# Optimization experiments

Measured on AMD Instinct MI355X. Metric: run time of the kernel, lower is better.

Reference implementation:

```python
import jax, jax.numpy as jnp
import numpy as np

N, E, DIN, DH, DC = 50000, 1600000, 128, 128, 40
EPS = 1e-5  # BatchNorm eps


def _seg_sum(v, idx, n):
    return jax.ops.segment_sum(v, idx, num_segments=n)


def setup_inputs() -> dict:
    key = jax.random.key(0)
    ks = jax.random.split(key, 24)
    rn = lambda i, shp, s=0.05: jax.random.normal(ks[i], shp, jnp.float32) * s
    return {
        "x": jax.random.normal(ks[0], (N, DIN), jnp.float32),
        "src": jax.random.randint(ks[1], (E,), 0, N, jnp.int32),
        "dst": jax.random.randint(ks[2], (E,), 0, N, jnp.int32),
        # CoNet layer 1 (in -> hidden)
        "w11s": rn(3, (DIN, DH)), "w11n": rn(4, (DIN, DH)), "b11": jnp.zeros((DH,), jnp.float32),
        "w12": rn(5, (DIN, DH)), "b12": jnp.zeros((DH,), jnp.float32),
        "w13": rn(6, (DIN, DH)), "a13l": rn(7, (DH,)), "a13r": rn(8, (DH,)), "b13": jnp.zeros((DH,), jnp.float32),
        "cw1": jax.random.uniform(ks[9], (3,), jnp.float32, 0.5, 1.5),
        # BatchNorm1d
        "g": jnp.ones((DH,), jnp.float32), "be": jnp.zeros((DH,), jnp.float32),
        # CoNet layer 2 (hidden -> out)
        "w21s": rn(10, (DH, DC)), "w21n": rn(11, (DH, DC)), "b21": jnp.zeros((DC,), jnp.float32),
        "w22": rn(12, (DH, DC)), "b22": jnp.zeros((DC,), jnp.float32),
        "w23": rn(13, (DH, DC)), "a23l": rn(14, (DC,)), "a23r": rn(15, (DC,)), "b23": jnp.zeros((DC,), jnp.float32),
        "cw2": jax.random.uniform(ks[16], (3,), jnp.float32, 0.5, 1.5),
    }


def conet(x, src, dst, ws, wn, bs, wg, bg, wa, al, ar, ba, cw):
    """AFFN CoNet: SAGE(mean) + GCN + GAT(1 head), fused by normalized weights."""
    n = x.shape[0]
    ones = jnp.ones((src.shape[0],), x.dtype)
    indeg = _seg_sum(ones, dst, n)   # in-degree per node
    outdeg = _seg_sum(ones, src, n)  # out-degree per node

    # --- SAGEConv, mean aggregator: fc_self(x) + fc_neigh(mean_neigh(x)) ---
    nei = _seg_sum(x[src], dst, n) / jnp.maximum(indeg, 1.0)[:, None]
    x1 = x @ ws + nei @ wn + bs

    ns = jnp.maximum(outdeg, 1.0) ** -0.5
    nd = jnp.maximum(indeg, 1.0) ** -0.5
    h = _seg_sum((x * ns[:, None])[src], dst, n) * nd[:, None]
    x2 = h @ wg + bg

    # --- GATConv, 1 head ---
    f = x @ wa                       # [N, out]
    el = f @ al                      # [N]
    er = f @ ar                      # [N]
    e = jax.nn.leaky_relu(el[src] + er[dst], 0.2)  # [E]
    m = jax.ops.segment_max(e, dst, num_segments=n)
    a = jnp.exp(e - m[dst])
    s = _seg_sum(a, dst, n)
    alpha = a / jnp.maximum(s[dst], 1e-9)
    x3 = _seg_sum(alpha[:, None] * f[src], dst, n) + ba

    w = cw / jnp.sum(cw)
    return w[0] * x1 + w[1] * x2 + w[2] * x3


def reference(x, src, dst,
              w11s, w11n, b11, w12, b12, w13, a13l, a13r, b13, cw1,
              g, be,
              w21s, w21n, b21, w22, b22, w23, a23l, a23r, b23, cw2):
    h = conet(x, src, dst, w11s, w11n, b11, w12, b12, w13, a13l, a13r, b13, cw1)
    # BatchNorm1d (training-mode batch statistics)
    mu = jnp.mean(h, axis=0)
    var = jnp.var(h, axis=0)
    h = (h - mu) * jax.lax.rsqrt(var + EPS) * g + be
    h = jax.nn.relu(h)
    # dropout in eval mode: identity
    h = conet(h, src, dst, w21s, w21n, b21, w22, b22, w23, a23l, a23r, b23, cw2)
    return jax.nn.log_softmax(h, axis=1)
```

## Files before the change

kernel.cpp:

```cpp
#include <hip/hip_runtime.h>
#include <hip/hip_bf16.h>
#include <math.h>

#define DIN 128
#define DH  128
#define DC  40

#define NSTRIPE 256
#define NPAD    50176
#define H8_WORDS (NPAD / 4)

typedef unsigned short u16;
typedef unsigned int u32;
typedef unsigned char u8;
typedef __attribute__((ext_vector_type(2))) float f32x2;
typedef __attribute__((ext_vector_type(4))) float f32x4;
typedef __attribute__((ext_vector_type(8))) short bf16x8;

static __device__ __forceinline__ float bf2f(u16 u) {
    union { u32 i; float f; } v; v.i = ((u32)u) << 16; return v.f;
}
static __device__ __forceinline__ u16 f2bf(float f) {
    __hip_bfloat16 h = __float2bfloat16(f);
    union { __hip_bfloat16 h; u16 u; } v; v.h = h; return v.u;
}
static __device__ __forceinline__ u32 pack2bf(float a, float b) {
    return ((u32)f2bf(b) << 16) | (u32)f2bf(a);
}
static __device__ __forceinline__ u32 cvtpk_bf16(float a, float b) {
    u32 r;
    asm("v_cvt_pk_bf16_f32 %0, %1, %2" : "=v"(r) : "v"(a), "v"(b));
    return r;
}

static __device__ __forceinline__ u8 f2fp8(float f) {
    u32 s = (__float_as_uint(f) >> 31) << 7;
    float a = fabsf(f);
    a = fminf(a, 448.f);
    if (a < 0.015625f) {
        int q = (int)rintf(a * 512.f);
        return (u8)(s | (u32)q);
    }
    u32 x = __float_as_uint(a);
    u32 lsb = (x >> 20) & 1;
    x += 0x0007FFFF + lsb;
    u32 e = (x >> 23) - 120;
    u32 m = (x >> 20) & 7;
    return (u8)(s | (e << 3) | m);
}

#if __has_builtin(__builtin_amdgcn_cvt_pk_f32_fp8)
template<bool HI>
static __device__ __forceinline__ f32x2 fp8pk(u32 w) {
    return __builtin_amdgcn_cvt_pk_f32_fp8((int)w, HI);
}
#else
static __device__ __forceinline__ float fp8dec1(u32 byte) {
    u32 s = (byte >> 7) & 1, em = byte & 0x7F;
    float v = __uint_as_float((s << 31) | (em << 20)) * 0x1p120f;
    return v;
}
template<bool HI>
static __device__ __forceinline__ f32x2 fp8pk(u32 w) {
    u32 b0 = HI ? ((w >> 16) & 0xff) : (w & 0xff);
    u32 b1 = HI ? ((w >> 24) & 0xff) : ((w >> 8) & 0xff);
    f32x2 r; r.x = fp8dec1(b0); r.y = fp8dec1(b1); return r;
}
#endif

__global__ __launch_bounds__(256) void k_prep(
        const float* w11s, const float* w11n, const float* w12, const float* w13,
        const float* b11, const float* b12, const float* b13, const float* cw1,
        const float* w21s, const float* w21n, const float* w22, const float* w23,
        const float* b21, const float* b22, const float* b23, const float* cw2,
        const float* a13l, const float* a13r, const float* a23l, const float* a23r,
        u16* __restrict__ Wf1, u16* __restrict__ Wf2,
        float* __restrict__ bc1, float* __restrict__ bc2, float* __restrict__ vattn,
        u32* __restrict__ zq, u32* __restrict__ zh) {
    int i = blockIdx.x * 256 + threadIdx.x;
    float s1 = cw1[0] + cw1[1] + cw1[2];
    float u0 = cw1[0] / s1, u1 = cw1[1] / s1, u2 = cw1[2] / s1;
    float s2 = cw2[0] + cw2[1] + cw2[2];
    float q0 = cw2[0] / s2, q1 = cw2[1] / s2, q2 = cw2[2] / s2;
    if (i < 65536) {
        int j = i & 7, lane = (i >> 3) & 63, nt = (i >> 9) & 7, kt = i >> 12;
        int k = kt * 32 + ((lane >> 4) << 3) + j;
        int n = nt * 16 + (lane & 15);
        float v;
        if (k < 128)      v = u0 * w11s[k * 128 + n];
        else if (k < 256) v = u0 * w11n[(k - 128) * 128 + n];
        else if (k < 384) v = u1 * w12[(k - 256) * 128 + n];
        else              v = u2 * w13[(k - 384) * 128 + n];
        Wf1[i] = f2bf(v);
    } else if (i < 90112) {
        int i2 = i - 65536;
        int j = i2 & 7;
        int l2 = i2 >> 3;
        int lane = l2 & 63;
        int t2 = l2 >> 6;
        int nt = t2 % 3, kt = t2 / 3;
        int k = kt * 32 + ((lane >> 4) << 3) + j;
        int n = nt * 16 + (lane & 15);
        float v = 0.f;
        if (n < 40) {
            if (k < 128)      v = q0 * w21s[k * 40 + n];
            else if (k < 256) v = q0 * w21n[(k - 128) * 40 + n];
            else if (k < 384) v = q1 * w22[(k - 256) * 40 + n];
            else              v = q2 * w23[(k - 384) * 40 + n];
        }
        Wf2[i2] = f2bf(v);
    } else if (i < 90624) {
        int t = i - 90112;
        if (t < 128) {
            float s = 0; for (int j = 0; j < 128; ++j) s += w13[t * 128 + j] * a13l[j];
            vattn[t] = s;
        } else if (t < 256) {
            int r = t - 128; float s = 0; for (int j = 0; j < 128; ++j) s += w13[r * 128 + j] * a13r[j];
            vattn[t] = s;
        } else if (t < 384) {
            int r = t - 256; float s = 0; for (int j = 0; j < 40; ++j) s += w23[r * 40 + j] * a23l[j];
            vattn[t] = s;
        } else {
            int r = t - 384; float s = 0; for (int j = 0; j < 40; ++j) s += w23[r * 40 + j] * a23r[j];
            vattn[t] = s;
        }
    } else if (i < 90752) {
        int c = i - 90624;
        bc1[c] = u0 * b11[c] + u1 * b12[c] + u2 * b13[c];
    } else if (i < 90792) {
        int c = i - 90752;
        bc2[c] = q0 * b21[c] + q1 * b22[c] + q2 * b23[c];
    } else if (i < 90856) {
        int t = i - 90792;
        if (t < 32) zq[t] = 0u; else zh[t - 32] = 0u;
    }
}

__global__ __launch_bounds__(512) void k_hist2(const int* __restrict__ src,
        const int* __restrict__ dst,
        u8* __restrict__ partialsS, u8* __restrict__ partialsD,
        u8* __restrict__ wsrank, int E, int eps) {
    __shared__ u32 histD[H8_WORDS];
    __shared__ u32 histS[H8_WORDS];
    int stripe = blockIdx.x;
    for (int i = threadIdx.x; i < H8_WORDS; i += 512) { histD[i] = 0; histS[i] = 0; }
    __syncthreads();
    int e0 = stripe * eps;
    int e1 = e0 + eps; if (e1 > E) e1 = E;
    for (int e = e0 + threadIdx.x; e < e1; e += 512) {
        int ks = src[e];
        int kd = dst[e];
        atomicAdd(&histS[ks >> 2], 1u << ((ks & 3) * 8));
        u32 old = atomicAdd(&histD[kd >> 2], 1u << ((kd & 3) * 8));
        wsrank[e] = (u8)((old >> ((kd & 3) * 8)) & 0xff);
    }
    __syncthreads();
    u32* prowS = (u32*)(partialsS + (size_t)stripe * NPAD);
    u32* prowD = (u32*)(partialsD + (size_t)stripe * NPAD);
    for (int i = threadIdx.x; i < H8_WORDS; i += 512) { prowD[i] = histD[i]; prowS[i] = histS[i]; }
}

__global__ __launch_bounds__(256) void k_pfx2(const u8* __restrict__ partialsS,
        u8* __restrict__ partialsD,
        int* __restrict__ excl, int* __restrict__ bsum,
        float* __restrict__ ns, int n) {
    int node = blockIdx.x * 256 + threadIdx.x;
    int runS = 0;
    for (int s0 = 0; s0 < NSTRIPE; s0 += 16) {
        u8 c[16];
#pragma unroll
        for (int i = 0; i < 16; ++i) c[i] = partialsS[(size_t)(s0 + i) * NPAD + node];
#pragma unroll
        for (int i = 0; i < 16; ++i) runS += c[i];
    }
    int runD = 0;
    for (int s0 = 0; s0 < NSTRIPE; s0 += 16) {
        u8 c[16];
#pragma unroll
        for (int i = 0; i < 16; ++i) c[i] = partialsD[(size_t)(s0 + i) * NPAD + node];
#pragma unroll
        for (int i = 0; i < 16; ++i) {
            partialsD[(size_t)(s0 + i) * NPAD + node] = (u8)runD;
            runD += c[i];
        }
    }
    if (node < n) {
        int d = runS < 1 ? 1 : runS;
        ns[node] = rsqrtf((float)d);
    }
    __shared__ int sh[256];
    sh[threadIdx.x] = runD; __syncthreads();
    for (int o = 1; o < 256; o <<= 1) {
        int t = (threadIdx.x >= o) ? sh[threadIdx.x - o] : 0;
        __syncthreads(); sh[threadIdx.x] += t; __syncthreads();
    }
    excl[node] = sh[threadIdx.x] - runD;
    if (threadIdx.x == 255) bsum[blockIdx.x] = sh[255];
}

__global__ __launch_bounds__(256) void k_place2(const int* __restrict__ src,
        const int* __restrict__ dst, const int* __restrict__ rowptr,
        const u8* __restrict__ partials, const u8* __restrict__ wsrank,
        int* __restrict__ col, int E, int eps) {
    int stripe = blockIdx.x;
    const u8* prow = partials + (size_t)stripe * NPAD;
    int sub = (eps + 3) >> 2;
    int e0 = stripe * eps + blockIdx.y * sub;
    int e1 = e0 + sub;
    int cap = stripe * eps + eps; if (cap > E) cap = E;
    if (e1 > cap) e1 = cap;
    for (int e = e0 + threadIdx.x; e < e1; e += 256) {
        int d = dst[e];
        col[rowptr[d] + prow[d] + wsrank[e]] = src[e];
    }
}

__global__ __launch_bounds__(256) void k_cvt_dots(const float* __restrict__ X,
        const float* __restrict__ vl, const float* __restrict__ vr, const float* __restrict__ ns,
        const int* __restrict__ excl, const int* __restrict__ bsum,
        u16* __restrict__ Xb, u8* __restrict__ Xq,
        float2* __restrict__ elns, float* __restrict__ er,
        int* __restrict__ rowptr, int n, int E, int pb) {
    __shared__ int sh[256], shE[256];
    int t = threadIdx.x;
    int v = (t < pb) ? bsum[t] : 0;
    sh[t] = v; __syncthreads();
    for (int o = 1; o < 256; o <<= 1) {
        int u = (t >= o) ? sh[t - o] : 0;
        __syncthreads(); sh[t] += u; __syncthreads();
    }
    shE[t] = sh[t] - v;
    __syncthreads();
    if (blockIdx.x == 0 && t == 0) rowptr[n] = E;
    int w = (blockIdx.x * blockDim.x + t) >> 6;
    int lane = t & 63;
    if (w >= n) return;
    float2 xv = *(const float2*)&X[(size_t)w * 128 + lane * 2];
    *(u32*)&Xb[(size_t)w * 128 + lane * 2] = cvtpk_bf16(xv.x, xv.y);
    u16 q = (u16)f2fp8(xv.x) | ((u16)f2fp8(xv.y) << 8);
    *(u16*)&Xq[(size_t)w * 128 + lane * 2] = q;
    float2 a = *(const float2*)&vl[lane * 2];
    float2 b = *(const float2*)&vr[lane * 2];
    float dl = xv.x * a.x + xv.y * a.y;
    float dr = xv.x * b.x + xv.y * b.y;
    for (int off = 32; off; off >>= 1) {
        dl += __shfl_down(dl, off);
        dr += __shfl_down(dr, off);
    }
    if (lane == 0) {
        rowptr[w] = excl[w] + shE[w >> 8];
        elns[w] = make_float2(dl, ns[w]);
        er[w] = dr;
    }
}

__global__ __launch_bounds__(256) void k_agg(const u8* __restrict__ Xq,
        const int* __restrict__ rowptr, const int* __restrict__ colsrc,
        const float2* __restrict__ elns, const float* __restrict__ er,
        u16* __restrict__ AG, int n) {
    int w = (blockIdx.x * blockDim.x + threadIdx.x) >> 6;
    int lane = threadIdx.x & 63;
    if (w >= n) return;
    int g = lane >> 4, gl = lane & 15;
    int beg = rowptr[w], end = rowptr[w + 1];
    int k = end - beg;
    float erd = er[w];
    f32x2 aS2[4] = {}, aG2[4] = {}, aA2[4] = {};
    float ssum_l = 0.f;
    for (int c0 = beg; c0 < end; c0 += 64) {
        int cnt = end - c0; if (cnt > 64) cnt = 64;
        int s = n; float p = 0.f; float nsl = 0.f;
        if (lane < cnt) {
            s = colsrc[c0 + lane];
            float2 v = elns[s];
            float t = v.x + erd;
            t = t > 0.f ? t : 0.2f * t;
            p = __expf(t);
            nsl = v.y;
        }
        ssum_l += p;
        int steps = (cnt + 3) >> 2;
#pragma unroll 8
        for (int t = 0; t < steps; ++t) {
            int j = (t << 2) + g;
            int sj = __shfl(s, j);
            float pj = __shfl(p, j);
            float nsj = __shfl(nsl, j);
            uint2 xq = *(const uint2*)&Xq[(size_t)sj * 128 + gl * 8];
            f32x2 xv2[4] = {fp8pk<false>(xq.x), fp8pk<true>(xq.x),
                            fp8pk<false>(xq.y), fp8pk<true>(xq.y)};
            f32x2 ns2 = {nsj, nsj}, p2 = {pj, pj};
#pragma unroll
            for (int q = 0; q < 4; ++q) {
                aS2[q] += xv2[q];
                aG2[q] += ns2 * xv2[q];
                aA2[q] += p2 * xv2[q];
            }
        }
    }
    for (int o = 32; o; o >>= 1) ssum_l += __shfl_xor(ssum_l, o);
    float aS[8], aG[8], aA[8];
#pragma unroll
    for (int i = 0; i < 4; ++i) {
        aS[2 * i] = aS2[i][0]; aS[2 * i + 1] = aS2[i][1];
        aG[2 * i] = aG2[i][0]; aG[2 * i + 1] = aG2[i][1];
        aA[2 * i] = aA2[i][0]; aA[2 * i + 1] = aA2[i][1];
    }
#pragma unroll
    for (int i = 0; i < 8; ++i) {
        aS[i] += __shfl_xor(aS[i], 16); aS[i] += __shfl_xor(aS[i], 32);
        aG[i] += __shfl_xor(aG[i], 16); aG[i] += __shfl_xor(aG[i], 32);
        aA[i] += __shfl_xor(aA[i], 16); aA[i] += __shfl_xor(aA[i], 32);
    }
    int kc = k < 1 ? 1 : k;
    float invk = 1.f / (float)kc;
    float ndd = rsqrtf((float)kc);
    float gi = 1.f / fmaxf(ssum_l, 1e-9f);
    u16* row = AG + (size_t)w * 384;
    if (g == 0) {
        uint4 o = make_uint4(pack2bf(aS[0] * invk, aS[1] * invk), pack2bf(aS[2] * invk, aS[3] * invk),
                             pack2bf(aS[4] * invk, aS[5] * invk), pack2bf(aS[6] * invk, aS[7] * invk));
        *(uint4*)&row[gl * 8] = o;
    } else if (g == 1) {
        uint4 o = make_uint4(pack2bf(aG[0] * ndd, aG[1] * ndd), pack2bf(aG[2] * ndd, aG[3] * ndd),
                             pack2bf(aG[4] * ndd, aG[5] * ndd), pack2bf(aG[6] * ndd, aG[7] * ndd));
        *(uint4*)&row[128 + gl * 8] = o;
    } else if (g == 2) {
        uint4 o = make_uint4(pack2bf(aA[0] * gi, aA[1] * gi), pack2bf(aA[2] * gi, aA[3] * gi),
                             pack2bf(aA[4] * gi, aA[5] * gi), pack2bf(aA[6] * gi, aA[7] * gi));
        *(uint4*)&row[256 + gl * 8] = o;
    }
}

__global__ __launch_bounds__(256) void k_gemm1(const u16* __restrict__ Xb,
        const u16* __restrict__ AG, const u16* __restrict__ Wf,
        const float* __restrict__ bias, u16* __restrict__ C,
        float* __restrict__ bnpart, int M) {
    const int NT = 8;
    int wave = threadIdx.x >> 6;
    int lane = threadIdx.x & 63;
    int m0 = blockIdx.x * 64 + wave * 16;
    int arow = m0 + (lane & 15);
    if (arow >= M) arow = M - 1;
    int kq = lane >> 4;
    f32x4 acc[NT];
#pragma unroll
    for (int t = 0; t < NT; ++t) acc[t] = (f32x4){0.f, 0.f, 0.f, 0.f};
#pragma unroll
    for (int kt = 0; kt < 16; ++kt) {
        int k0 = kt * 32 + kq * 8;
        bf16x8 a;
        if (k0 < 128) a = *(const bf16x8*)&Xb[(size_t)arow * 128 + k0];
        else          a = *(const bf16x8*)&AG[(size_t)arow * 384 + (k0 - 128)];
        const u16* wb = Wf + ((size_t)kt * NT) * 512 + lane * 8;
#pragma unroll
        for (int t = 0; t < NT; ++t) {
            bf16x8 b = *(const bf16x8*)&wb[(size_t)t * 512];
            acc[t] = __builtin_amdgcn_mfma_f32_16x16x32_bf16(a, b, acc[t], 0, 0, 0);
        }
    }
    __shared__ float sS[128], sQ[128];
    if (threadIdx.x < 128) { sS[threadIdx.x] = 0.f; sQ[threadIdx.x] = 0.f; }
    __syncthreads();
    int ccol = lane & 15;
    int rbase = m0 + kq * 4;
#pragma unroll
    for (int t = 0; t < NT; ++t) {
        int col = t * 16 + ccol;
        float bv = bias[col];
        float cs = 0.f, cq = 0.f;
#pragma unroll
        for (int r = 0; r < 4; ++r) {
            int rr = rbase + r;
            float v = acc[t][r] + bv;
            if (rr < M) {
                C[(size_t)rr * 128 + col] = f2bf(v);
                cs += v; cq += v * v;
            }
        }
        cs += __shfl_xor(cs, 16); cs += __shfl_xor(cs, 32);
        cq += __shfl_xor(cq, 16); cq += __shfl_xor(cq, 32);
        if (kq == 0) {
            atomicAdd(&sS[col], cs);
            atomicAdd(&sQ[col], cq);
        }
    }
    __syncthreads();
    if (threadIdx.x < 128) {
        bnpart[(size_t)blockIdx.x * 256 + threadIdx.x] = sS[threadIdx.x];
        bnpart[(size_t)blockIdx.x * 256 + 128 + threadIdx.x] = sQ[threadIdx.x];
    }
}

__global__ __launch_bounds__(256) void k_bn_reduce(const float* __restrict__ bnpart,
                                                   float* __restrict__ bnacc, int nb) {
    int c = blockIdx.x;
    float s = 0.f;
    for (int r = threadIdx.x; r < nb; r += 256)
        s += bnpart[(size_t)r * 256 + c];
    for (int o = 32; o; o >>= 1) s += __shfl_xor(s, o);
    __shared__ float sw[4];
    if ((threadIdx.x & 63) == 0) sw[threadIdx.x >> 6] = s;
    __syncthreads();
    if (threadIdx.x == 0) bnacc[c] = sw[0] + sw[1] + sw[2] + sw[3];
}

__global__ __launch_bounds__(256) void k_gemm2_lsm(const u16* __restrict__ Xb,
        const u16* __restrict__ AG, const u16* __restrict__ Wf,
        const float* __restrict__ bias, float* __restrict__ out, int M) {
    const int NT = 3;
    int wave = threadIdx.x >> 6;
    int lane = threadIdx.x & 63;
    int m0 = blockIdx.x * 64 + wave * 16;
    int arow = m0 + (lane & 15);
    if (arow >= M) arow = M - 1;
    int kq = lane >> 4;
    f32x4 acc[NT];
#pragma unroll
    for (int t = 0; t < NT; ++t) acc[t] = (f32x4){0.f, 0.f, 0.f, 0.f};
#pragma unroll
    for (int kt = 0; kt < 16; ++kt) {
        int k0 = kt * 32 + kq * 8;
        bf16x8 a;
        if (k0 < 128) a = *(const bf16x8*)&Xb[(size_t)arow * 128 + k0];
        else          a = *(const bf16x8*)&AG[(size_t)arow * 384 + (k0 - 128)];
        const u16* wb = Wf + ((size_t)kt * NT) * 512 + lane * 8;
#pragma unroll
        for (int t = 0; t < NT; ++t) {
            bf16x8 b = *(const bf16x8*)&wb[(size_t)t * 512];
            acc[t] = __builtin_amdgcn_mfma_f32_16x16x32_bf16(a, b, acc[t], 0, 0, 0);
        }
    }
    int ccol = lane & 15;
    int rbase = m0 + kq * 4;
    bool valid[NT];
    float bv[NT];
#pragma unroll
    for (int t = 0; t < NT; ++t) {
        int col = t * 16 + ccol;
        valid[t] = (col < 40);
        bv[t] = valid[t] ? bias[col] : 0.f;
    }
#pragma unroll
    for (int r = 0; r < 4; ++r) {
        float v[NT];
#pragma unroll
        for (int t = 0; t < NT; ++t) v[t] = valid[t] ? (acc[t][r] + bv[t]) : -INFINITY;
        float mx = fmaxf(fmaxf(v[0], v[1]), v[2]);
        for (int o = 1; o < 16; o <<= 1) mx = fmaxf(mx, __shfl_xor(mx, o));
        float se = 0.f;
#pragma unroll
        for (int t = 0; t < NT; ++t) se += valid[t] ? __expf(v[t] - mx) : 0.f;
        for (int o = 1; o < 16; o <<= 1) se += __shfl_xor(se, o);
        float lse = mx + logf(se);
        int rr = rbase + r;
        if (rr < M) {
#pragma unroll
            for (int t = 0; t < NT; ++t) {
                int col = t * 16 + ccol;
                if (valid[t]) out[(size_t)rr * 40 + col] = v[t] - lse;
            }
        }
    }
}

__global__ __launch_bounds__(256) void k_bnorm_dots(const u16* __restrict__ Hp,
        const float* __restrict__ bnacc, const float* __restrict__ g, const float* __restrict__ be,
        const float* __restrict__ vl, const float* __restrict__ vr,
        const float* __restrict__ ns,
        u16* __restrict__ H, u8* __restrict__ H8,
        float2* __restrict__ elns, float* __restrict__ er, float Nf, int n) {
    int w = (blockIdx.x * blockDim.x + threadIdx.x) >> 6;
    int lane = threadIdx.x & 63;
    if (w >= n) return;
    int c0 = lane * 2, c1 = lane * 2 + 1;
    float mu0 = bnacc[c0] / Nf, mu1 = bnacc[c1] / Nf;
    float var0 = bnacc[128 + c0] / Nf - mu0 * mu0;
    float var1 = bnacc[128 + c1] / Nf - mu1 * mu1;
    float sc0 = g[c0] * rsqrtf(var0 + 1e-5f);
    float sc1 = g[c1] * rsqrtf(var1 + 1e-5f);
    float sh0 = be[c0] - mu0 * sc0;
    float sh1 = be[c1] - mu1 * sc1;
    u32 hu = *(const u32*)&Hp[(size_t)w * 128 + lane * 2];
    float vx = bf2f((u16)hu), vy = bf2f((u16)(hu >> 16));
    float h0 = fmaxf(vx * sc0 + sh0, 0.f);
    float h1 = fmaxf(vy * sc1 + sh1, 0.f);
    *(u32*)&H[(size_t)w * 128 + lane * 2] = cvtpk_bf16(h0, h1);
    u16 q = (u16)f2fp8(h0) | ((u16)f2fp8(h1) << 8);
    *(u16*)&H8[(size_t)w * 128 + lane * 2] = q;
    float2 a = *(const float2*)&vl[lane * 2];
    float2 b = *(const float2*)&vr[lane * 2];
    float dl = h0 * a.x + h1 * a.y;
    float dr = h0 * b.x + h1 * b.y;
    for (int off = 32; off; off >>= 1) {
        dl += __shfl_down(dl, off);
        dr += __shfl_down(dr, off);
    }
    if (lane == 0) { elns[w] = make_float2(dl, ns[w]); er[w] = dr; }
}

extern "C" void kernel_launch(void* const* d_in, const int* in_sizes, int n_in,
                              void* d_out, int out_size, void* d_ws, size_t ws_size,
                              hipStream_t stream) {
    const float* x    = (const float*)d_in[0];
    const int*   src  = (const int*)d_in[1];
    const int*   dst  = (const int*)d_in[2];
    const float* w11s = (const float*)d_in[3];
    const float* w11n = (const float*)d_in[4];
    const float* b11  = (const float*)d_in[5];
    const float* w12  = (const float*)d_in[6];
    const float* b12  = (const float*)d_in[7];
    const float* w13  = (const float*)d_in[8];
    const float* a13l = (const float*)d_in[9];
    const float* a13r = (const float*)d_in[10];
    const float* b13  = (const float*)d_in[11];
    const float* cw1  = (const float*)d_in[12];
    const float* g    = (const float*)d_in[13];
    const float* be   = (const float*)d_in[14];
    const float* w21s = (const float*)d_in[15];
    const float* w21n = (const float*)d_in[16];
    const float* b21  = (const float*)d_in[17];
    const float* w22  = (const float*)d_in[18];
    const float* b22  = (const float*)d_in[19];
    const float* w23  = (const float*)d_in[20];
    const float* a23l = (const float*)d_in[21];
    const float* a23r = (const float*)d_in[22];
    const float* b23  = (const float*)d_in[23];
    const float* cw2  = (const float*)d_in[24];

    const int N = in_sizes[0] / DIN;
    const int E = in_sizes[1];

    char* ws = (char*)d_ws;
    size_t off = 0;
    auto alloc = [&](size_t bytes) { size_t o = off; off += (bytes + 255) & ~(size_t)255; return o; };
    u16*   Xb     = (u16*)(ws + alloc((size_t)N * 128 * 2));
    u8*    Xq     = (u8*)(ws + alloc((size_t)(N + 1) * 128));
    u16*   AG     = (u16*)(ws + alloc((size_t)N * 384 * 2));
    u16*   hpre   = (u16*)(ws + alloc((size_t)N * 128 * 2));
    u16*   h      = (u16*)(ws + alloc((size_t)N * 128 * 2));
    u8*    h8     = (u8*)(ws + alloc((size_t)(N + 1) * 128));
    int*   col    = (int*)(ws + alloc((size_t)E * 4));
    u8*    wsrank = (u8*)(ws + alloc((size_t)E));
    int*   rowptr = (int*)(ws + alloc((size_t)(N + 1) * 4));
    int*   excl   = (int*)(ws + alloc((size_t)NPAD * 4));
    int*   bsum   = (int*)(ws + alloc(256 * 4));
    float* ns     = (float*)(ws + alloc((size_t)N * 4));
    float2* elns  = (float2*)(ws + alloc((size_t)N * 8));
    float* er     = (float*)(ws + alloc((size_t)N * 4));
    u16*   Wf1    = (u16*)(ws + alloc((size_t)16 * 8 * 64 * 8 * 2));
    u16*   Wf2    = (u16*)(ws + alloc((size_t)16 * 3 * 64 * 8 * 2));
    float* bc1    = (float*)(ws + alloc(128 * 4));
    float* bc2    = (float*)(ws + alloc(40 * 4));
    float* vattn  = (float*)(ws + alloc(512 * 4));
    float* bnacc  = (float*)(ws + alloc(256 * 4));
    float* bnpart = (float*)(ws + alloc((size_t)((N + 63) / 64) * 256 * 4));

    u8* partialsS = (u8*)AG;
    u8* partialsD = (u8*)hpre;

    int eps = (E + NSTRIPE - 1) / NSTRIPE;
    int wb = (N * 64 + 255) / 256;
    int gb = (N + 63) / 64;
    int pb = NPAD / 256;

    k_prep<<<(90856 + 255) / 256, 256, 0, stream>>>(
        w11s, w11n, w12, w13, b11, b12, b13, cw1,
        w21s, w21n, w22, w23, b21, b22, b23, cw2,
        a13l, a13r, a23l, a23r, Wf1, Wf2, bc1, bc2, vattn,
        (u32*)(Xq + (size_t)N * 128), (u32*)(h8 + (size_t)N * 128));

    k_hist2<<<NSTRIPE, 512, 0, stream>>>(src, dst, partialsS, partialsD, wsrank, E, eps);
    k_pfx2<<<pb, 256, 0, stream>>>(partialsS, partialsD, excl, bsum, ns, N);

    k_cvt_dots<<<wb, 256, 0, stream>>>(x, vattn, vattn + 128, ns, excl, bsum,
                                       Xb, Xq, elns, er, rowptr, N, E, pb);
    {
        dim3 pg(NSTRIPE, 4);
        k_place2<<<pg, 256, 0, stream>>>(src, dst, rowptr, partialsD, wsrank, col, E, eps);
    }

    k_agg<<<wb, 256, 0, stream>>>(Xq, rowptr, col, elns, er, AG, N);
    k_gemm1<<<gb, 256, 0, stream>>>(Xb, AG, Wf1, bc1, hpre, bnpart, N);

    k_bn_reduce<<<256, 256, 0, stream>>>(bnpart, bnacc, gb);
    k_bnorm_dots<<<wb, 256, 0, stream>>>(hpre, bnacc, g, be, vattn + 256, vattn + 384, ns,
                                         h, h8, elns, er, (float)N, N);

    k_agg<<<wb, 256, 0, stream>>>(h8, rowptr, col, elns, er, AG, N);
    k_gemm2_lsm<<<gb, 256, 0, stream>>>(h, AG, Wf2, bc2, (float*)d_out, N);
}
```

Baseline: 378.0 us.

## Assign one 16-lane group per destination node in edge aggregation

The aggregation kernel now gives each 16-lane quarter-wave its own destination node instead of giving a whole wave one node. Each quarter loads up to 16 neighbor indices at a time and loops to the largest degree among the wave's four nodes. This removes the cross-group shuffle reductions at the end and cuts the grid to a quarter of its former size. The trade-off is lost lanes when the four nodes in a wave have uneven degrees, and fewer independent loads in flight per node.

New measurement: 366.2 us, median of 2. 3.1% less time.

```diff
diff --git a/kernel.cpp b/kernel.cpp
--- a/kernel.cpp
+++ b/kernel.cpp
@@ -258,20 +258,25 @@
         const int* __restrict__ rowptr, const int* __restrict__ colsrc,
         const float2* __restrict__ elns, const float* __restrict__ er,
         u16* __restrict__ AG, int n) {
-    int w = (blockIdx.x * blockDim.x + threadIdx.x) >> 6;
+    int wave = (blockIdx.x * blockDim.x + threadIdx.x) >> 6;
     int lane = threadIdx.x & 63;
-    if (w >= n) return;
     int g = lane >> 4, gl = lane & 15;
-    int beg = rowptr[w], end = rowptr[w + 1];
+    int w = wave * 4 + g;
+    bool act = (w < n);
+    int beg = 0, end = 0;
+    if (act) { beg = rowptr[w]; end = rowptr[w + 1]; }
     int k = end - beg;
-    float erd = er[w];
+    float erd = act ? er[w] : 0.f;
+    int kmax = k;
+    kmax = max(kmax, __shfl_xor(kmax, 16));
+    kmax = max(kmax, __shfl_xor(kmax, 32));
     f32x2 aS2[4] = {}, aG2[4] = {}, aA2[4] = {};
     float ssum_l = 0.f;
-    for (int c0 = beg; c0 < end; c0 += 64) {
-        int cnt = end - c0; if (cnt > 64) cnt = 64;
-        int s = n; float p = 0.f; float nsl = 0.f;
-        if (lane < cnt) {
-            s = colsrc[c0 + lane];
+    for (int c = 0; c < kmax; c += 16) {
+        int cnt = k - c; cnt = cnt < 0 ? 0 : (cnt > 16 ? 16 : cnt);
+        int s = n; float p = 0.f, nsl = 0.f;
+        if (gl < cnt) {
+            s = colsrc[beg + c + gl];
             float2 v = elns[s];
             float t = v.x + erd;
             t = t > 0.f ? t : 0.2f * t;
@@ -279,10 +284,10 @@
             nsl = v.y;
         }
         ssum_l += p;
-        int steps = (cnt + 3) >> 2;
+        int cm = kmax - c; if (cm > 16) cm = 16;
 #pragma unroll 8
-        for (int t = 0; t < steps; ++t) {
-            int j = (t << 2) + g;
+        for (int t = 0; t < cm; ++t) {
+            int j = (g << 4) + t;
             int sj = __shfl(s, j);
             float pj = __shfl(p, j);
             float nsj = __shfl(nsl, j);
@@ -298,38 +303,31 @@
             }
         }
     }
-    for (int o = 32; o; o >>= 1) ssum_l += __shfl_xor(ssum_l, o);
-    float aS[8], aG[8], aA[8];
-#pragma unroll
-    for (int i = 0; i < 4; ++i) {
-        aS[2 * i] = aS2[i][0]; aS[2 * i + 1] = aS2[i][1];
-        aG[2 * i] = aG2[i][0]; aG[2 * i + 1] = aG2[i][1];
-        aA[2 * i] = aA2[i][0]; aA[2 * i + 1] = aA2[i][1];
-    }
-#pragma unroll
-    for (int i = 0; i < 8; ++i) {
-        aS[i] += __shfl_xor(aS[i], 16); aS[i] += __shfl_xor(aS[i], 32);
-        aG[i] += __shfl_xor(aG[i], 16); aG[i] += __shfl_xor(aG[i], 32);
-        aA[i] += __shfl_xor(aA[i], 16); aA[i] += __shfl_xor(aA[i], 32);
-    }
+    ssum_l += __shfl_xor(ssum_l, 1);
+    ssum_l += __shfl_xor(ssum_l, 2);
+    ssum_l += __shfl_xor(ssum_l, 4);
+    ssum_l += __shfl_xor(ssum_l, 8);
+    if (!act) return;
     int kc = k < 1 ? 1 : k;
     float invk = 1.f / (float)kc;
     float ndd = rsqrtf((float)kc);
     float gi = 1.f / fmaxf(ssum_l, 1e-9f);
     u16* row = AG + (size_t)w * 384;
-    if (g == 0) {
-        uint4 o = make_uint4(pack2bf(aS[0] * invk, aS[1] * invk), pack2bf(aS[2] * invk, aS[3] * invk),
-                             pack2bf(aS[4] * invk, aS[5] * invk), pack2bf(aS[6] * invk, aS[7] * invk));
-        *(uint4*)&row[gl * 8] = o;
-    } else if (g == 1) {
-        uint4 o = make_uint4(pack2bf(aG[0] * ndd, aG[1] * ndd), pack2bf(aG[2] * ndd, aG[3] * ndd),
-                             pack2bf(aG[4] * ndd, aG[5] * ndd), pack2bf(aG[6] * ndd, aG[7] * ndd));
-        *(uint4*)&row[128 + gl * 8] = o;
-    } else if (g == 2) {
-        uint4 o = make_uint4(pack2bf(aA[0] * gi, aA[1] * gi), pack2bf(aA[2] * gi, aA[3] * gi),
-                             pack2bf(aA[4] * gi, aA[5] * gi), pack2bf(aA[6] * gi, aA[7] * gi));
-        *(uint4*)&row[256 + gl * 8] = o;
-    }
+    uint2 oS = make_uint2(pack2bf(aS2[0][0] * invk, aS2[0][1] * invk),
+                          pack2bf(aS2[1][0] * invk, aS2[1][1] * invk));
+    uint2 oS2 = make_uint2(pack2bf(aS2[2][0] * invk, aS2[2][1] * invk),
+                           pack2bf(aS2[3][0] * invk, aS2[3][1] * invk));
+    *(uint4*)&row[gl * 8] = make_uint4(oS.x, oS.y, oS2.x, oS2.y);
+    uint2 oG = make_uint2(pack2bf(aG2[0][0] * ndd, aG2[0][1] * ndd),
+                          pack2bf(aG2[1][0] * ndd, aG2[1][1] * ndd));
+    uint2 oG2 = make_uint2(pack2bf(aG2[2][0] * ndd, aG2[2][1] * ndd),
+                           pack2bf(aG2[3][0] * ndd, aG2[3][1] * ndd));
+    *(uint4*)&row[128 + gl * 8] = make_uint4(oG.x, oG.y, oG2.x, oG2.y);
+    uint2 oA = make_uint2(pack2bf(aA2[0][0] * gi, aA2[0][1] * gi),
+                          pack2bf(aA2[1][0] * gi, aA2[1][1] * gi));
+    uint2 oA2 = make_uint2(pack2bf(aA2[2][0] * gi, aA2[2][1] * gi),
+                           pack2bf(aA2[3][0] * gi, aA2[3][1] * gi));
+    *(uint4*)&row[256 + gl * 8] = make_uint4(oA.x, oA.y, oA2.x, oA2.y);
 }
 
 __global__ __launch_bounds__(256) void k_gemm1(const u16* __restrict__ Xb,
@@ -561,6 +559,7 @@
 
     int eps = (E + NSTRIPE - 1) / NSTRIPE;
     int wb = (N * 64 + 255) / 256;
+    int ab = (N + 15) / 16;
     int gb = (N + 63) / 64;
     int pb = NPAD / 256;
 
@@ -580,13 +579,13 @@
         k_place2<<<pg, 256, 0, stream>>>(src, dst, rowptr, partialsD, wsrank, col, E, eps);
     }
 
-    k_agg<<<wb, 256, 0, stream>>>(Xq, rowptr, col, elns, er, AG, N);
+    k_agg<<<ab, 256, 0, stream>>>(Xq, rowptr, col, elns, er, AG, N);
     k_gemm1<<<gb, 256, 0, stream>>>(Xb, AG, Wf1, bc1, hpre, bnpart, N);
 
     k_bn_reduce<<<256, 256, 0, stream>>>(bnpart, bnacc, gb);
     k_bnorm_dots<<<wb, 256, 0, stream>>>(hpre, bnacc, g, be, vattn + 256, vattn + 384, ns,
                                          h, h8, elns, er, (float)N, N);
 
-    k_agg<<<wb, 256, 0, stream>>>(h8, rowptr, col, elns, er, AG, N);
+    k_agg<<<ab, 256, 0, stream>>>(h8, rowptr, col, elns, er, AG, N);
     k_gemm2_lsm<<<gb, 256, 0, stream>>>(h, AG, Wf2, bc2, (float*)d_out, N);
 }
```
